# Performance work log

Hardware: AMD Instinct MI355X
Metric: run time of the kernel (lower is better)

The kernel has to match this reference:

```python
import jax, jax.numpy as jnp
import numpy as np

N_NODES = 50000


def setup_inputs() -> dict:
    key = jax.random.key(0)
    ks = jax.random.split(key, 6)
    nfeat, nhid, hops, nedges = 256, 64, 4, 800000
    x = jax.random.normal(ks[0], (N_NODES, nfeat), dtype=jnp.float32)
    W = jax.random.normal(ks[1], (hops, nfeat, nhid), dtype=jnp.float32) / np.sqrt(nfeat)
    b = jax.random.normal(ks[2], (hops, nhid), dtype=jnp.float32) * 0.01
    adj_rows = jax.random.randint(ks[3], (hops, nedges), 0, N_NODES, dtype=jnp.int32)
    adj_cols = jax.random.randint(ks[4], (hops, nedges), 0, N_NODES, dtype=jnp.int32)
    # normalize-ish positive edge weights, as in a GCN-normalized adjacency
    adj_vals = jax.random.uniform(ks[5], (hops, nedges), dtype=jnp.float32) / 16.0
    return {"x": x, "W": W, "b": b, "adj_rows": adj_rows,
            "adj_cols": adj_cols, "adj_vals": adj_vals}


def reference(x, W, b, adj_rows, adj_cols, adj_vals):
    # SIGN forward (eval mode: dropout = identity).
    # For each hop i: h = x @ W[i] + b[i]; out_i = spmm(adj_i, h)
    # spmm in COO form: out[r] = sum_{e: rows[e]==r} vals[e] * h[cols[e]]
    n = x.shape[0]
    hops = W.shape[0]
    outs = []
    for i in range(hops):  # small fixed hop count (layers+1)
        h = x @ W[i] + b[i]                      # [N, nhid] dense GEMM
        msgs = adj_vals[i][:, None] * h[adj_cols[i]]  # [E, nhid] gather
        outs.append(jax.ops.segment_sum(msgs, adj_rows[i], num_segments=n))
    return jax.nn.elu(jnp.concatenate(outs, axis=1))  # [N, hops*nhid]
```

## Files before the change

### kernel.cpp

```cpp
#include <hip/hip_runtime.h>
#include <hip/hip_bf16.h>
#include <math.h>

#define N_NODES 50000
#define NFEAT 256
#define NHID 64
#define HOPS 4
#define NEDGES 800000
#define NBINS (HOPS * N_NODES)

#define BROWS 64
#define NBUCK 782
#define NBK_ALL (HOPS * NBUCK)
#define CHUNK 4096
#define NCHUNK ((NEDGES + CHUNK - 1) / CHUNK)
#define FS_CAP 2048
#define MCAP 512

#define GM 64
#define LDP 40
#define NGBLK ((N_NODES + GM - 1) / GM)

typedef short bf16x8 __attribute__((ext_vector_type(8)));
typedef float f32x4 __attribute__((ext_vector_type(4)));

static __device__ __forceinline__ unsigned short f2bf(float f) {
    __hip_bfloat16 h = __float2bfloat16(f);
    return *reinterpret_cast<unsigned short*>(&h);
}

__global__ __launch_bounds__(256) void castx_kernel(const float* __restrict__ x,
                                                    unsigned short* __restrict__ Xbf) {
    const int i = blockIdx.x * 256 + threadIdx.x;
    const size_t base = (size_t)i * 8;
    if (base < (size_t)N_NODES * NFEAT) {
        const float4 a = *(const float4*)&x[base];
        const float4 c = *(const float4*)&x[base + 4];
        unsigned short o[8] = {f2bf(a.x), f2bf(a.y), f2bf(a.z), f2bf(a.w),
                               f2bf(c.x), f2bf(c.y), f2bf(c.z), f2bf(c.w)};
        *(bf16x8*)&Xbf[base] = *(const bf16x8*)o;
    }
}

__global__ __launch_bounds__(256) void castw_kernel(const float* __restrict__ W,
                                                    unsigned short* __restrict__ Wt) {
    const int idx = blockIdx.x * 256 + threadIdx.x;
    if (idx < HOPS * NFEAT * NHID) {
        const int hop = idx >> 14;
        const int k = (idx >> 6) & 255;
        const int c = idx & 63;
        Wt[((size_t)(hop * 64 + c)) * NFEAT + k] = f2bf(W[idx]);
    }
}

__global__ __launch_bounds__(256) void gemm_bf_kernel(const unsigned short* __restrict__ Xbf,
                                                      const unsigned short* __restrict__ Wt,
                                                      const float* __restrict__ b,
                                                      __hip_bfloat16* __restrict__ H) {
    __shared__ unsigned short A_lds[GM * LDP];
    __shared__ unsigned short B_lds[256 * LDP];

    const int t = threadIdx.x;
    const int lane = t & 63;
    const int w = t >> 6;
    const int quad = lane >> 4;
    const int m16 = lane & 15;
    const int row0 = blockIdx.x * GM;

    f32x4 acc[4][4];
#pragma unroll
    for (int mt = 0; mt < 4; ++mt)
#pragma unroll
        for (int nt = 0; nt < 4; ++nt) acc[mt][nt] = (f32x4){0.f, 0.f, 0.f, 0.f};

    for (int ks = 0; ks < 8; ++ks) {
        const int k0 = ks * 32;
        {
            const int r = t >> 2;
            const int kq = (t & 3) * 8;
            bf16x8 v = {0, 0, 0, 0, 0, 0, 0, 0};
            if (row0 + r < N_NODES)
                v = *(const bf16x8*)&Xbf[(size_t)(row0 + r) * NFEAT + k0 + kq];
            *(bf16x8*)&A_lds[r * LDP + kq] = v;
        }
#pragma unroll
        for (int q = 0; q < 4; ++q) {
            const int kq = q * 8;
            const bf16x8 v = *(const bf16x8*)&Wt[(size_t)t * NFEAT + k0 + kq];
            *(bf16x8*)&B_lds[t * LDP + kq] = v;
        }
        __syncthreads();

        bf16x8 af[4], bf[4];
#pragma unroll
        for (int mt = 0; mt < 4; ++mt)
            af[mt] = *(const bf16x8*)&A_lds[(mt * 16 + m16) * LDP + quad * 8];
#pragma unroll
        for (int nt = 0; nt < 4; ++nt)
            bf[nt] = *(const bf16x8*)&B_lds[(w * 64 + nt * 16 + m16) * LDP + quad * 8];
#pragma unroll
        for (int mt = 0; mt < 4; ++mt)
#pragma unroll
            for (int nt = 0; nt < 4; ++nt)
                acc[mt][nt] = __builtin_amdgcn_mfma_f32_16x16x32_bf16(
                    af[mt], bf[nt], acc[mt][nt], 0, 0, 0);
        __syncthreads();
    }

#pragma unroll
    for (int nt = 0; nt < 4; ++nt) {
        const int col = w * 64 + nt * 16 + m16;
        const float bias = b[col];
#pragma unroll
        for (int mt = 0; mt < 4; ++mt) {
#pragma unroll
            for (int r = 0; r < 4; ++r) {
                const int row = row0 + mt * 16 + quad * 4 + r;
                if (row < N_NODES)
                    H[(size_t)row * 256 + col] = __float2bfloat16(acc[mt][nt][r] + bias);
            }
        }
    }
}

__global__ __launch_bounds__(256) void gemm_mfma_kernel(const float* __restrict__ x,
                                                        const float* __restrict__ W,
                                                        const float* __restrict__ b,
                                                        __hip_bfloat16* __restrict__ H) {
    __shared__ unsigned short A_lds[GM * LDP];
    __shared__ unsigned short B_lds[256 * LDP];

    const int t = threadIdx.x;
    const int lane = t & 63;
    const int w = t >> 6;
    const int quad = lane >> 4;
    const int m16 = lane & 15;
    const int row0 = blockIdx.x * GM;

    f32x4 acc[4][4];
#pragma unroll
    for (int mt = 0; mt < 4; ++mt)
#pragma unroll
        for (int nt = 0; nt < 4; ++nt) acc[mt][nt] = (f32x4){0.f, 0.f, 0.f, 0.f};

    for (int ks = 0; ks < 8; ++ks) {
        const int k0 = ks * 32;
#pragma unroll
        for (int it = 0; it < 2; ++it) {
            const int i = t + it * 256;
            const int r = i >> 3;
            const int kq = (i & 7) * 4;
            float4 v = make_float4(0.f, 0.f, 0.f, 0.f);
            if (row0 + r < N_NODES)
                v = *(const float4*)&x[(size_t)(row0 + r) * NFEAT + k0 + kq];
            unsigned short* d = &A_lds[r * LDP + kq];
            d[0] = f2bf(v.x); d[1] = f2bf(v.y); d[2] = f2bf(v.z); d[3] = f2bf(v.w);
        }
#pragma unroll
        for (int it = 0; it < 8; ++it) {
            const int i = t + it * 256;
            const int n4 = i & 63;
            const int kk = i >> 6;
            const int hop = n4 >> 4;
            const int j = (n4 & 15) * 4;
            const float4 v = *(const float4*)&W[(size_t)hop * (NFEAT * NHID)
                                                + (size_t)(k0 + kk) * NHID + j];
            B_lds[(n4 * 4 + 0) * LDP + kk] = f2bf(v.x);
            B_lds[(n4 * 4 + 1) * LDP + kk] = f2bf(v.y);
            B_lds[(n4 * 4 + 2) * LDP + kk] = f2bf(v.z);
            B_lds[(n4 * 4 + 3) * LDP + kk] = f2bf(v.w);
        }
        __syncthreads();

        bf16x8 af[4], bf[4];
#pragma unroll
        for (int mt = 0; mt < 4; ++mt)
            af[mt] = *(const bf16x8*)&A_lds[(mt * 16 + m16) * LDP + quad * 8];
#pragma unroll
        for (int nt = 0; nt < 4; ++nt)
            bf[nt] = *(const bf16x8*)&B_lds[(w * 64 + nt * 16 + m16) * LDP + quad * 8];
#pragma unroll
        for (int mt = 0; mt < 4; ++mt)
#pragma unroll
            for (int nt = 0; nt < 4; ++nt)
                acc[mt][nt] = __builtin_amdgcn_mfma_f32_16x16x32_bf16(
                    af[mt], bf[nt], acc[mt][nt], 0, 0, 0);
        __syncthreads();
    }

#pragma unroll
    for (int nt = 0; nt < 4; ++nt) {
        const int col = w * 64 + nt * 16 + m16;
        const float bias = b[col];
#pragma unroll
        for (int mt = 0; mt < 4; ++mt) {
#pragma unroll
            for (int r = 0; r < 4; ++r) {
                const int row = row0 + mt * 16 + quad * 4 + r;
                if (row < N_NODES)
                    H[(size_t)row * 256 + col] = __float2bfloat16(acc[mt][nt][r] + bias);
            }
        }
    }
}

__global__ __launch_bounds__(256) void bhist_kernel(const int* __restrict__ rows,
                                                    int* __restrict__ bucket_cnt) {
    __shared__ int h[NBUCK];
    const int t = threadIdx.x;
    for (int i = t; i < NBUCK; i += 256) h[i] = 0;
    __syncthreads();
    const int hop = blockIdx.y;
    const int e0 = blockIdx.x * CHUNK;
    const int n = min(CHUNK, NEDGES - e0);
    const size_t base = (size_t)hop * NEDGES + e0;
    for (int i = t; i < n; i += 256) {
        atomicAdd(&h[rows[base + i] >> 6], 1);
    }
    __syncthreads();
    for (int i = t; i < NBUCK; i += 256) {
        if (h[i]) atomicAdd(&bucket_cnt[hop * NBUCK + i], h[i]);
    }
}

#define SCAN_V ((NBK_ALL + 255) / 256)
__global__ __launch_bounds__(256) void bscan_kernel(const int* __restrict__ cnt,
                                                    int* __restrict__ start,
                                                    int* __restrict__ cursor,
                                                    int* __restrict__ offsets) {
    __shared__ int s[256];
    const int t = threadIdx.x;
    int v[SCAN_V];
    int tsum = 0;
#pragma unroll
    for (int i = 0; i < SCAN_V; ++i) {
        const int idx = t * SCAN_V + i;
        v[i] = (idx < NBK_ALL) ? cnt[idx] : 0;
        tsum += v[i];
    }
    s[t] = tsum;
    __syncthreads();
    for (int off = 1; off < 256; off <<= 1) {
        const int a = (t >= off) ? s[t - off] : 0;
        __syncthreads();
        s[t] += a;
        __syncthreads();
    }
    int run = s[t] - tsum;
#pragma unroll
    for (int i = 0; i < SCAN_V; ++i) {
        const int idx = t * SCAN_V + i;
        if (idx < NBK_ALL) {
            start[idx] = run;
            cursor[idx] = run;
            run += v[i];
        }
    }
    if (t == 255) {
        start[NBK_ALL] = run;
        offsets[NBINS] = run;
    }
}

__global__ __launch_bounds__(256) void partition_kernel(const int* __restrict__ rows,
                                                        const int* __restrict__ cols,
                                                        const float* __restrict__ vals,
                                                        int* __restrict__ cursor,
                                                        int2* __restrict__ partbuf) {
    __shared__ int2 pay[CHUNK];
    __shared__ int h[NBUCK], excl[NBUCK], gbase[NBUCK], lcur[NBUCK];
    __shared__ int s[256];
    const int t = threadIdx.x;
    const int hop = blockIdx.y;
    const int e0 = blockIdx.x * CHUNK;
    const int n = min(CHUNK, NEDGES - e0);
    const size_t base = (size_t)hop * NEDGES + e0;

    for (int i = t; i < NBUCK; i += 256) h[i] = 0;
    __syncthreads();

    int myrow[CHUNK / 256];
#pragma unroll
    for (int j = 0; j < CHUNK / 256; ++j) {
        const int i = t + j * 256;
        if (i < n) {
            const int r = rows[base + i];
            myrow[j] = r;
            atomicAdd(&h[r >> 6], 1);
        }
    }
    __syncthreads();

    int pv[4];
    int tsum = 0;
#pragma unroll
    for (int i = 0; i < 4; ++i) {
        const int idx = t * 4 + i;
        pv[i] = (idx < NBUCK) ? h[idx] : 0;
        tsum += pv[i];
    }
    s[t] = tsum;
    __syncthreads();
    for (int off = 1; off < 256; off <<= 1) {
        const int a = (t >= off) ? s[t - off] : 0;
        __syncthreads();
        s[t] += a;
        __syncthreads();
    }
    int run = s[t] - tsum;
#pragma unroll
    for (int i = 0; i < 4; ++i) {
        const int idx = t * 4 + i;
        if (idx < NBUCK) {
            excl[idx] = run;
            lcur[idx] = run;
            gbase[idx] = pv[i] ? atomicAdd(&cursor[hop * NBUCK + idx], pv[i]) : 0;
            run += pv[i];
        }
    }
    __syncthreads();

#pragma unroll
    for (int j = 0; j < CHUNK / 256; ++j) {
        const int i = t + j * 256;
        if (i < n) {
            const int r = myrow[j];
            const int c = cols[base + i];
            const float v = vals[base + i];
            const int pos = atomicAdd(&lcur[r >> 6], 1);
            pay[pos] = make_int2((r << 16) | c, __float_as_int(v));
        }
    }
    __syncthreads();

    for (int i = t; i < n; i += 256) {
        const int2 p = pay[i];
        const int bk = ((unsigned)p.x) >> 22;
        partbuf[gbase[bk] + (i - excl[bk])] = p;
    }
}

__global__ __launch_bounds__(256) void fsort_kernel(const int* __restrict__ start,
                                                    int2* __restrict__ partbuf,
                                                    int* __restrict__ offsets) {
    __shared__ int2 pay[FS_CAP];
    __shared__ int h[BROWS], excl[BROWS], cur[BROWS];
    __shared__ int s[256];
    const int t = threadIdx.x;
    const int hop = blockIdx.y;
    const int bucket = blockIdx.x;
    const int g = hop * NBUCK + bucket;
    const int s0 = start[g];
    const int n = min(start[g + 1] - s0, FS_CAP);

    if (t < BROWS) h[t] = 0;
    __syncthreads();

    for (int i = t; i < n; i += 256) {
        const int2 p = partbuf[s0 + i];
        pay[i] = p;
        atomicAdd(&h[((unsigned)p.x >> 16) & (BROWS - 1)], 1);
    }
    __syncthreads();

    const int hv = (t < BROWS) ? h[t] : 0;
    s[t] = hv;
    __syncthreads();
    for (int off = 1; off < 256; off <<= 1) {
        const int a = (t >= off) ? s[t - off] : 0;
        __syncthreads();
        s[t] += a;
        __syncthreads();
    }
    if (t < BROWS) {
        const int ex = s[t] - hv;
        excl[t] = ex;
        cur[t] = 0;
        const int row = bucket * BROWS + t;
        if (row < N_NODES) offsets[hop * N_NODES + row] = s0 + ex;
    }
    __syncthreads();

    for (int i = t; i < n; i += 256) {
        const int2 p = pay[i];
        const int rl = ((unsigned)p.x >> 16) & (BROWS - 1);
        const int pos = s0 + excl[rl] + atomicAdd(&cur[rl], 1);
        partbuf[pos] = make_int2(p.x & 0xFFFF, p.y);
    }
}

__global__ __launch_bounds__(256) void csr_gather_kernel(const __hip_bfloat16* __restrict__ H,
                                                         const int* __restrict__ offsets,
                                                         const int2* __restrict__ epk,
                                                         float* __restrict__ out) {
    __shared__ int2 meta[4][MCAP + 8];
    const int t = threadIdx.x;
    const int f = t & 63;
    const int w = t >> 6;
    const int hop = blockIdx.y;
    const int row0w = blockIdx.x * 64 + w * 16;
    if (row0w >= N_NODES) return;
    const int bin0 = hop * N_NODES + row0w;

    int off_l = 0;
    if (f <= 16) off_l = offsets[bin0 + f];
    const int s0w = __builtin_amdgcn_readlane(off_l, 0);
    const int s1w = __builtin_amdgcn_readlane(off_l, 16);
    const int cnt = s1w - s0w;

    const unsigned short* Hf = (const unsigned short*)H + hop * 64 + f;
    float* outp = out + (size_t)row0w * 256 + hop * 64 + f;

    if (cnt <= MCAP) {
        int2* M = meta[w];
        for (int i = f; i < cnt; i += 64) M[i] = epk[s0w + i];
        if (f < 8) M[cnt + f] = make_int2(0, 0);

        for (int r = 0; r < 16; ++r) {
            const int s  = __builtin_amdgcn_readlane(off_l, r) - s0w;
            const int e2 = __builtin_amdgcn_readlane(off_l, r + 1) - s0w;
            float acc = 0.f;
            for (int g = s; g < e2; g += 8) {
                int2 mm[8];
#pragma unroll
                for (int j = 0; j < 8; ++j) mm[j] = M[g + j];
                float h8[8];
#pragma unroll
                for (int j = 0; j < 8; ++j)
                    h8[j] = __uint_as_float(
                        (unsigned)Hf[(size_t)(unsigned)mm[j].x << 8] << 16);
#pragma unroll
                for (int j = 0; j < 8; ++j) {
                    const float vj = (g + j < e2) ? __int_as_float(mm[j].y) : 0.f;
                    acc = fmaf(vj, h8[j], acc);
                }
            }
            acc = acc > 0.f ? acc : expf(acc) - 1.f;
            outp[(size_t)r * 256] = acc;
        }
    } else {
        for (int r = 0; r < 16; ++r) {
            const int s  = __builtin_amdgcn_readlane(off_l, r);
            const int e2 = __builtin_amdgcn_readlane(off_l, r + 1);
            float acc = 0.f;
            int e = s;
            for (; e + 8 <= e2; e += 8) {
                const int2 m = epk[e + (f & 7)];
                float h8[8];
#pragma unroll
                for (int j = 0; j < 8; ++j) {
                    const int col = __builtin_amdgcn_readlane(m.x, j);
                    h8[j] = __uint_as_float((unsigned)Hf[(size_t)col << 8] << 16);
                }
#pragma unroll
                for (int j = 0; j < 8; ++j) {
                    const float val =
                        __uint_as_float((unsigned)__builtin_amdgcn_readlane(m.y, j));
                    acc = fmaf(val, h8[j], acc);
                }
            }
            if (e < e2) {
                const int2 m = epk[e + (f & 7)];
                const int rem = e2 - e;
                for (int j = 0; j < rem; ++j) {
                    const int col = __builtin_amdgcn_readlane(m.x, j);
                    const float val =
                        __uint_as_float((unsigned)__builtin_amdgcn_readlane(m.y, j));
                    acc = fmaf(val, __uint_as_float((unsigned)Hf[(size_t)col << 8] << 16),
                               acc);
                }
            }
            acc = acc > 0.f ? acc : expf(acc) - 1.f;
            outp[(size_t)r * 256] = acc;
        }
    }
}

#define EPW 8
__global__ __launch_bounds__(256) void scatter_kernel(const __hip_bfloat16* __restrict__ H,
                                                      const int* __restrict__ rows,
                                                      const int* __restrict__ cols,
                                                      const float* __restrict__ vals,
                                                      float* __restrict__ out) {
    const int lane = threadIdx.x & 63;
    const int wid = __builtin_amdgcn_readfirstlane(threadIdx.x >> 6);
    const int hop = blockIdx.y;
    const int e0 = (blockIdx.x * 4 + wid) * EPW;
    const int base = hop * NEDGES;
    const int hoff = hop * 64 + lane;
#pragma unroll
    for (int i = 0; i < EPW; ++i) {
        const int e = e0 + i;
        const int r = rows[base + e];
        const int c = cols[base + e];
        const float v = vals[base + e];
        unsafeAtomicAdd(&out[(size_t)r * 256 + hoff],
                        v * __bfloat162float(H[(size_t)c * 256 + hoff]));
    }
}

__global__ __launch_bounds__(256) void elu_kernel(float* __restrict__ out, int n4) {
    const int i = blockIdx.x * 256 + threadIdx.x;
    if (i < n4) {
        float4 v = ((float4*)out)[i];
        v.x = v.x > 0.f ? v.x : expf(v.x) - 1.f;
        v.y = v.y > 0.f ? v.y : expf(v.y) - 1.f;
        v.z = v.z > 0.f ? v.z : expf(v.z) - 1.f;
        v.w = v.w > 0.f ? v.w : expf(v.w) - 1.f;
        ((float4*)out)[i] = v;
    }
}

extern "C" void kernel_launch(void* const* d_in, const int* in_sizes, int n_in,
                              void* d_out, int out_size, void* d_ws, size_t ws_size,
                              hipStream_t stream) {
    const float* x        = (const float*)d_in[0];
    const float* W        = (const float*)d_in[1];
    const float* b        = (const float*)d_in[2];
    const int*   adj_rows = (const int*)d_in[3];
    const int*   adj_cols = (const int*)d_in[4];
    const float* adj_vals = (const float*)d_in[5];
    float* out = (float*)d_out;

    char* w = (char*)d_ws;
    size_t off = 0;
    __hip_bfloat16* H = (__hip_bfloat16*)(w + off);
    off += (size_t)N_NODES * 256 * 2;
    int2*  partbuf    = (int2*)(w + off);  off += (size_t)HOPS * NEDGES * 8;
    int*   offsets    = (int*)(w + off);   off += (((size_t)(NBINS + 1)) * 4 + 255) & ~255ull;
    int*   bucket_cnt = (int*)(w + off);   off += ((size_t)NBK_ALL * 4 + 255) & ~255ull;
    int*   bstart     = (int*)(w + off);   off += (((size_t)NBK_ALL + 1) * 4 + 255) & ~255ull;
    int*   bcursor    = (int*)(w + off);   off += ((size_t)NBK_ALL * 4 + 255) & ~255ull;
    const bool use_sorted = (ws_size >= off);

    unsigned short* Xbf = (unsigned short*)partbuf;
    unsigned short* Wt  = (unsigned short*)offsets;

    if (use_sorted) {
        castx_kernel<<<(N_NODES * NFEAT / 8 + 255) / 256, 256, 0, stream>>>(x, Xbf);
        castw_kernel<<<(HOPS * NFEAT * NHID + 255) / 256, 256, 0, stream>>>(W, Wt);
        gemm_bf_kernel<<<NGBLK, 256, 0, stream>>>(Xbf, Wt, b, H);

        hipMemsetAsync(bucket_cnt, 0, (size_t)NBK_ALL * 4, stream);
        bhist_kernel<<<dim3(NCHUNK, HOPS), 256, 0, stream>>>(adj_rows, bucket_cnt);
        bscan_kernel<<<1, 256, 0, stream>>>(bucket_cnt, bstart, bcursor, offsets);
        partition_kernel<<<dim3(NCHUNK, HOPS), 256, 0, stream>>>(adj_rows, adj_cols,
                                                                 adj_vals, bcursor, partbuf);
        fsort_kernel<<<dim3(NBUCK, HOPS), 256, 0, stream>>>(bstart, partbuf, offsets);
        csr_gather_kernel<<<dim3((N_NODES + 63) / 64, HOPS), 256, 0, stream>>>(
            H, offsets, partbuf, out);
    } else {
        gemm_mfma_kernel<<<NGBLK, 256, 0, stream>>>(x, W, b, H);
        hipMemsetAsync(d_out, 0, (size_t)out_size * sizeof(float), stream);
        scatter_kernel<<<dim3(NEDGES / (4 * EPW), HOPS), 256, 0, stream>>>(
            H, adj_rows, adj_cols, adj_vals, out);
        elu_kernel<<<(out_size / 4 + 255) / 256, 256, 0, stream>>>(out, out_size / 4);
    }
}
```

Measured before the change: 336.6 us.

## Fuse prep and scan launches; widen CSR gather to bf16 pairs per lane

Merges the bucket histogram, W cast and x cast into one prep_kernel that dispatches work by block index. It also folds the bucket scan into the GEMM launch as an extra block 0, cutting the launch count and the gaps between small kernels. In the short-row CSR gather path, each lane now loads two adjacent bf16 features with one 32-bit load, and the two half-waves take alternate groups of 8 edges. Their partial sums are combined with a cross-half shuffle. This issues fewer, wider gather loads and handles 16 edges per iteration, at the cost of the extra shuffle and half the lanes sitting idle on the store.

```diff
diff --git a/kernel.cpp b/kernel.cpp
--- a/kernel.cpp
+++ b/kernel.cpp
@@ -21,6 +21,11 @@
 #define LDP 40
 #define NGBLK ((N_NODES + GM - 1) / GM)
 
+#define PREP_BHIST (NCHUNK * HOPS)
+#define PREP_CASTW_END (PREP_BHIST + 256)
+#define PREP_CASTX_BLKS ((N_NODES * NFEAT / 8) / 256)
+#define PREP_TOTAL (PREP_CASTW_END + PREP_CASTX_BLKS)
+
 typedef short bf16x8 __attribute__((ext_vector_type(8)));
 typedef float f32x4 __attribute__((ext_vector_type(4)));
 
@@ -29,11 +34,38 @@
     return *reinterpret_cast<unsigned short*>(&h);
 }
 
-__global__ __launch_bounds__(256) void castx_kernel(const float* __restrict__ x,
-                                                    unsigned short* __restrict__ Xbf) {
-    const int i = blockIdx.x * 256 + threadIdx.x;
-    const size_t base = (size_t)i * 8;
-    if (base < (size_t)N_NODES * NFEAT) {
+__global__ __launch_bounds__(256) void prep_kernel(const float* __restrict__ x,
+                                                   unsigned short* __restrict__ Xbf,
+                                                   const float* __restrict__ W,
+                                                   unsigned short* __restrict__ Wt,
+                                                   const int* __restrict__ rows,
+                                                   int* __restrict__ bucket_cnt) {
+    __shared__ int h[NBUCK];
+    const int bid = blockIdx.x;
+    const int t = threadIdx.x;
+
+    if (bid < PREP_BHIST) {
+        for (int i = t; i < NBUCK; i += 256) h[i] = 0;
+        __syncthreads();
+        const int hop = bid / NCHUNK;
+        const int e0 = (bid % NCHUNK) * CHUNK;
+        const int n = min(CHUNK, NEDGES - e0);
+        const size_t base = (size_t)hop * NEDGES + e0;
+        for (int i = t; i < n; i += 256) {
+            atomicAdd(&h[rows[base + i] >> 6], 1);
+        }
+        __syncthreads();
+        for (int i = t; i < NBUCK; i += 256) {
+            if (h[i]) atomicAdd(&bucket_cnt[hop * NBUCK + i], h[i]);
+        }
+    } else if (bid < PREP_CASTW_END) {
+        const int idx = (bid - PREP_BHIST) * 256 + t;
+        const int hop = idx >> 14;
+        const int k = (idx >> 6) & 255;
+        const int c = idx & 63;
+        Wt[((size_t)(hop * 64 + c)) * NFEAT + k] = f2bf(W[idx]);
+    } else {
+        const size_t base = ((size_t)(bid - PREP_CASTW_END) * 256 + t) * 8;
         const float4 a = *(const float4*)&x[base];
         const float4 c = *(const float4*)&x[base + 4];
         unsigned short o[8] = {f2bf(a.x), f2bf(a.y), f2bf(a.z), f2bf(a.w),
@@ -42,30 +74,61 @@
     }
 }
 
-__global__ __launch_bounds__(256) void castw_kernel(const float* __restrict__ W,
-                                                    unsigned short* __restrict__ Wt) {
-    const int idx = blockIdx.x * 256 + threadIdx.x;
-    if (idx < HOPS * NFEAT * NHID) {
-        const int hop = idx >> 14;
-        const int k = (idx >> 6) & 255;
-        const int c = idx & 63;
-        Wt[((size_t)(hop * 64 + c)) * NFEAT + k] = f2bf(W[idx]);
-    }
-}
-
-__global__ __launch_bounds__(256) void gemm_bf_kernel(const unsigned short* __restrict__ Xbf,
-                                                      const unsigned short* __restrict__ Wt,
-                                                      const float* __restrict__ b,
-                                                      __hip_bfloat16* __restrict__ H) {
-    __shared__ unsigned short A_lds[GM * LDP];
-    __shared__ unsigned short B_lds[256 * LDP];
-
+#define SCAN_V ((NBK_ALL + 255) / 256)
+__global__ __launch_bounds__(256) void gemm_scan_kernel(const unsigned short* __restrict__ Xbf,
+                                                        const unsigned short* __restrict__ Wt,
+                                                        const float* __restrict__ b,
+                                                        __hip_bfloat16* __restrict__ H,
+                                                        const int* __restrict__ cnt,
+                                                        int* __restrict__ start,
+                                                        int* __restrict__ cursor,
+                                                        int* __restrict__ offsets) {
+    __shared__ char smem[GM * LDP * 2 + 256 * LDP * 2];
     const int t = threadIdx.x;
+
+    if (blockIdx.x == 0) {
+        int* s = (int*)smem;
+        int v[SCAN_V];
+        int tsum = 0;
+#pragma unroll
+        for (int i = 0; i < SCAN_V; ++i) {
+            const int idx = t * SCAN_V + i;
+            v[i] = (idx < NBK_ALL) ? cnt[idx] : 0;
+            tsum += v[i];
+        }
+        s[t] = tsum;
+        __syncthreads();
+        for (int off = 1; off < 256; off <<= 1) {
+            const int a = (t >= off) ? s[t - off] : 0;
+            __syncthreads();
+            s[t] += a;
+            __syncthreads();
+        }
+        int run = s[t] - tsum;
+#pragma unroll
+        for (int i = 0; i < SCAN_V; ++i) {
+            const int idx = t * SCAN_V + i;
+            if (idx < NBK_ALL) {
+                start[idx] = run;
+                cursor[idx] = run;
+                run += v[i];
+            }
+        }
+        if (t == 255) {
+            start[NBK_ALL] = run;
+            offsets[NBINS] = run;
+        }
+        return;
+    }
+
+    unsigned short* A_lds = (unsigned short*)smem;
+    unsigned short* B_lds = (unsigned short*)(smem + GM * LDP * 2);
+
     const int lane = t & 63;
     const int w = t >> 6;
     const int quad = lane >> 4;
     const int m16 = lane & 15;
-    const int row0 = blockIdx.x * GM;
+    const int row0 = (blockIdx.x - 1) * GM;
 
     f32x4 acc[4][4];
 #pragma unroll
@@ -201,64 +264,6 @@
                     H[(size_t)row * 256 + col] = __float2bfloat16(acc[mt][nt][r] + bias);
             }
         }
-    }
-}
-
-__global__ __launch_bounds__(256) void bhist_kernel(const int* __restrict__ rows,
-                                                    int* __restrict__ bucket_cnt) {
-    __shared__ int h[NBUCK];
-    const int t = threadIdx.x;
-    for (int i = t; i < NBUCK; i += 256) h[i] = 0;
-    __syncthreads();
-    const int hop = blockIdx.y;
-    const int e0 = blockIdx.x * CHUNK;
-    const int n = min(CHUNK, NEDGES - e0);
-    const size_t base = (size_t)hop * NEDGES + e0;
-    for (int i = t; i < n; i += 256) {
-        atomicAdd(&h[rows[base + i] >> 6], 1);
-    }
-    __syncthreads();
-    for (int i = t; i < NBUCK; i += 256) {
-        if (h[i]) atomicAdd(&bucket_cnt[hop * NBUCK + i], h[i]);
-    }
-}
-
-#define SCAN_V ((NBK_ALL + 255) / 256)
-__global__ __launch_bounds__(256) void bscan_kernel(const int* __restrict__ cnt,
-                                                    int* __restrict__ start,
-                                                    int* __restrict__ cursor,
-                                                    int* __restrict__ offsets) {
-    __shared__ int s[256];
-    const int t = threadIdx.x;
-    int v[SCAN_V];
-    int tsum = 0;
-#pragma unroll
-    for (int i = 0; i < SCAN_V; ++i) {
-        const int idx = t * SCAN_V + i;
-        v[i] = (idx < NBK_ALL) ? cnt[idx] : 0;
-        tsum += v[i];
-    }
-    s[t] = tsum;
-    __syncthreads();
-    for (int off = 1; off < 256; off <<= 1) {
-        const int a = (t >= off) ? s[t - off] : 0;
-        __syncthreads();
-        s[t] += a;
-        __syncthreads();
-    }
-    int run = s[t] - tsum;
-#pragma unroll
-    for (int i = 0; i < SCAN_V; ++i) {
-        const int idx = t * SCAN_V + i;
-        if (idx < NBK_ALL) {
-            start[idx] = run;
-            cursor[idx] = run;
-            run += v[i];
-        }
-    }
-    if (t == 255) {
-        start[NBK_ALL] = run;
-        offsets[NBINS] = run;
     }
 }
 
@@ -393,7 +398,7 @@
                                                          const int* __restrict__ offsets,
                                                          const int2* __restrict__ epk,
                                                          float* __restrict__ out) {
-    __shared__ int2 meta[4][MCAP + 8];
+    __shared__ int2 meta[4][MCAP + 16];
     const int t = threadIdx.x;
     const int f = t & 63;
     const int w = t >> 6;
@@ -408,37 +413,46 @@
     const int s1w = __builtin_amdgcn_readlane(off_l, 16);
     const int cnt = s1w - s0w;
 
-    const unsigned short* Hf = (const unsigned short*)H + hop * 64 + f;
-    float* outp = out + (size_t)row0w * 256 + hop * 64 + f;
-
     if (cnt <= MCAP) {
+        const int gi = f >> 5;
+        const int fp = f & 31;
+        const char* Hb = (const char*)H + hop * 128 + fp * 4;
+        float* outp = out + (size_t)row0w * 256 + hop * 64 + fp * 2;
+
         int2* M = meta[w];
         for (int i = f; i < cnt; i += 64) M[i] = epk[s0w + i];
-        if (f < 8) M[cnt + f] = make_int2(0, 0);
+        if (f < 16) M[cnt + f] = make_int2(0, 0);
 
         for (int r = 0; r < 16; ++r) {
             const int s  = __builtin_amdgcn_readlane(off_l, r) - s0w;
             const int e2 = __builtin_amdgcn_readlane(off_l, r + 1) - s0w;
-            float acc = 0.f;
-            for (int g = s; g < e2; g += 8) {
+            float aLo = 0.f, aHi = 0.f;
+            for (int g = s; g < e2; g += 16) {
                 int2 mm[8];
 #pragma unroll
-                for (int j = 0; j < 8; ++j) mm[j] = M[g + j];
-                float h8[8];
-#pragma unroll
-                for (int j = 0; j < 8; ++j)
-                    h8[j] = __uint_as_float(
-                        (unsigned)Hf[(size_t)(unsigned)mm[j].x << 8] << 16);
+                for (int j = 0; j < 8; ++j) mm[j] = M[g + gi * 8 + j];
+                unsigned hv[8];
 #pragma unroll
                 for (int j = 0; j < 8; ++j) {
-                    const float vj = (g + j < e2) ? __int_as_float(mm[j].y) : 0.f;
-                    acc = fmaf(vj, h8[j], acc);
+                    hv[j] = *(const unsigned*)(Hb + ((size_t)(unsigned)mm[j].x << 9));
+                }
+#pragma unroll
+                for (int j = 0; j < 8; ++j) {
+                    const float vj = (g + gi * 8 + j < e2) ? __int_as_float(mm[j].y) : 0.f;
+                    aLo = fmaf(vj, __uint_as_float(hv[j] << 16), aLo);
+                    aHi = fmaf(vj, __uint_as_float(hv[j] & 0xffff0000u), aHi);
                 }
             }
-            acc = acc > 0.f ? acc : expf(acc) - 1.f;
-            outp[(size_t)r * 256] = acc;
+            aLo += __shfl_xor(aLo, 32, 64);
+            aHi += __shfl_xor(aHi, 32, 64);
+            aLo = aLo > 0.f ? aLo : expf(aLo) - 1.f;
+            aHi = aHi > 0.f ? aHi : expf(aHi) - 1.f;
+            if (f < 32)
+                *(float2*)(outp + (size_t)r * 256) = make_float2(aLo, aHi);
         }
     } else {
+        const unsigned short* Hf = (const unsigned short*)H + hop * 64 + f;
+        float* outp = out + (size_t)row0w * 256 + hop * 64 + f;
         for (int r = 0; r < 16; ++r) {
             const int s  = __builtin_amdgcn_readlane(off_l, r);
             const int e2 = __builtin_amdgcn_readlane(off_l, r + 1);
@@ -537,13 +551,10 @@
     unsigned short* Wt  = (unsigned short*)offsets;
 
     if (use_sorted) {
-        castx_kernel<<<(N_NODES * NFEAT / 8 + 255) / 256, 256, 0, stream>>>(x, Xbf);
-        castw_kernel<<<(HOPS * NFEAT * NHID + 255) / 256, 256, 0, stream>>>(W, Wt);
-        gemm_bf_kernel<<<NGBLK, 256, 0, stream>>>(Xbf, Wt, b, H);
-
         hipMemsetAsync(bucket_cnt, 0, (size_t)NBK_ALL * 4, stream);
-        bhist_kernel<<<dim3(NCHUNK, HOPS), 256, 0, stream>>>(adj_rows, bucket_cnt);
-        bscan_kernel<<<1, 256, 0, stream>>>(bucket_cnt, bstart, bcursor, offsets);
+        prep_kernel<<<PREP_TOTAL, 256, 0, stream>>>(x, Xbf, W, Wt, adj_rows, bucket_cnt);
+        gemm_scan_kernel<<<NGBLK + 1, 256, 0, stream>>>(Xbf, Wt, b, H,
+                                                        bucket_cnt, bstart, bcursor, offsets);
         partition_kernel<<<dim3(NCHUNK, HOPS), 256, 0, stream>>>(adj_rows, adj_cols,
                                                                  adj_vals, bcursor, partbuf);
         fsort_kernel<<<dim3(NBUCK, HOPS), 256, 0, stream>>>(bstart, partbuf, offsets);
```

New measurement: 321.5 us. 1.05x faster.
